# Kernel tuning notes

Measured on AMD Instinct MI355X. Metric: run time of the kernel, lower is better.

The kernel has to match this reference:

```python
import jax, jax.numpy as jnp
import numpy as np

EPS = 1e-6
N_REP = 4  # num_heads // num_kv_heads


def _qk_norm(a):
    a32 = a.astype(jnp.float32)
    var = jnp.mean(jnp.square(a32), axis=-1, keepdims=True)
    return (a32 * jax.lax.rsqrt(var + EPS)).astype(a.dtype)


def setup_inputs() -> dict:
    key = jax.random.key(0)
    ks = jax.random.split(key, 5)
    B, Tq, C, H, D, Hkv = 2, 2048, 2048, 16, 128, 4
    s = 0.02
    return {
        "x_q": jax.random.normal(ks[0], (B, Tq, C), dtype=jnp.float32),
        "Wq": jax.random.normal(ks[1], (C, H, D), dtype=jnp.float32) * s,
        "Wk": jax.random.normal(ks[2], (C, Hkv, D), dtype=jnp.float32) * s,
        "Wv": jax.random.normal(ks[3], (C, Hkv, D), dtype=jnp.float32) * s,
        "Wo": jax.random.normal(ks[4], (H * D, C), dtype=jnp.float32) * s,
    }


def reference(x_q, Wq, Wk, Wv, Wo):
    # x_q: (B, Tq, C); self-attention (x_kv = x_q)
    B, Tq, C = x_q.shape
    D = Wq.shape[-1]
    q = jnp.einsum('btc,chd->bthd', x_q, Wq)   # (B,Tq,H,D)
    k = jnp.einsum('btc,chd->bthd', x_q, Wk)   # (B,Tq,Hkv,D)
    v = jnp.einsum('btc,chd->bthd', x_q, Wv)
    # per-head QK RMS-norm
    q = _qk_norm(q)
    k = _qk_norm(k)
    # GQA: repeat kv heads (each kv head repeated N_REP times consecutively)
    k = jnp.repeat(k, N_REP, axis=2)           # (B,Tq,H,D)
    v = jnp.repeat(v, N_REP, axis=2)
    scale = jnp.asarray(1.0 / np.sqrt(D), dtype=q.dtype)
    logits = jnp.einsum('bqhd,bkhd->bhqk', q, k) * scale
    attn = jax.nn.softmax(logits, axis=-1)
    out = jnp.einsum('bhqk,bkhd->bqhd', attn, v)
    out = out.reshape(B, Tq, -1)               # (B,Tq,H*D)
    return out @ Wo                            # (B,Tq,C)
```

## Files before the change

### kernel.cpp

```cpp
#include <hip/hip_runtime.h>

typedef __attribute__((ext_vector_type(4))) float f32x4;
typedef __attribute__((ext_vector_type(16))) float f32x16;
typedef __attribute__((ext_vector_type(8))) short bf16x8;
typedef __attribute__((ext_vector_type(4))) unsigned u32x4;

#define DEV __device__ __forceinline__

DEV unsigned short f2bf(float f) {
  unsigned u = __float_as_uint(f);
  unsigned r = (u + 0x7FFFu + ((u >> 16) & 1u)) >> 16;
  return (unsigned short)r;
}
DEV float bf2f(unsigned short h) { return __uint_as_float(((unsigned)h) << 16); }

DEV unsigned cvtpk(float lo, float hi) {
  unsigned r;
  asm("v_cvt_pk_bf16_f32 %0, %1, %2" : "=v"(r) : "v"(lo), "v"(hi));
  return r;
}
DEV bf16x8 frag4(unsigned a, unsigned b, unsigned c, unsigned d) {
  u32x4 u = {a, b, c, d};
  return __builtin_bit_cast(bf16x8, u);
}

typedef __attribute__((address_space(1))) void gas_t;
typedef __attribute__((address_space(3))) void las_t;
DEV void async16(void* lds, const void* g) {
  __builtin_amdgcn_global_load_lds((gas_t*)g, (las_t*)lds, 16, 0, 0);
}

__global__ void cast_x(const float* __restrict__ x, unsigned short* __restrict__ y, int n8) {
  int idx = blockIdx.x * blockDim.x + threadIdx.x;
  int stride = gridDim.x * blockDim.x;
  for (; idx < n8; idx += stride) {
    const float4* p = (const float4*)(x + (size_t)idx * 8);
    float4 v0 = p[0], v1 = p[1];
    bf16x8 o;
    o[0] = (short)f2bf(v0.x); o[1] = (short)f2bf(v0.y);
    o[2] = (short)f2bf(v0.z); o[3] = (short)f2bf(v0.w);
    o[4] = (short)f2bf(v1.x); o[5] = (short)f2bf(v1.y);
    o[6] = (short)f2bf(v1.z); o[7] = (short)f2bf(v1.w);
    *(bf16x8*)(y + (size_t)idx * 8) = o;
  }
}

__global__ void transpose_cast(const float* __restrict__ W, unsigned short* __restrict__ Wt,
                               int Kdim, int Nw) {
  __shared__ float tile[32][33];
  int n0 = blockIdx.x * 32, k0 = blockIdx.y * 32;
  int tx = threadIdx.x, ty = threadIdx.y;
#pragma unroll
  for (int r = ty; r < 32; r += 8)
    tile[r][tx] = W[(size_t)(k0 + r) * Nw + n0 + tx];
  __syncthreads();
#pragma unroll
  for (int r = ty; r < 32; r += 8)
    Wt[(size_t)(n0 + r) * Kdim + k0 + tx] = f2bf(tile[tx][r]);
}

template <int EPI>
__global__ __launch_bounds__(256, 3)
void gemm_bt(const unsigned short* __restrict__ A, const unsigned short* __restrict__ Bt,
             int Kr, float* __restrict__ Cf, int Nr,
             unsigned short* __restrict__ Qn, unsigned short* __restrict__ Kn,
             unsigned short* __restrict__ Vt, float qscale) {
  __shared__ __align__(16) unsigned short lsA[128 * 32];
  __shared__ __align__(16) unsigned short lsB[128 * 32];
  const int t = threadIdx.x;
  const int lane = t & 63;
  const int w = t >> 6, wr = w >> 1, wc = w & 1;
  const int lo = lane & 15, hi = lane >> 4;
  const int nwg = gridDim.x * 32;
  const int bid0 = blockIdx.y * gridDim.x + blockIdx.x;
  const int sw = (bid0 & 7) * (nwg >> 3) + (bid0 >> 3);
  const int m0 = (sw & 31) * 128, n0 = (sw >> 5) * 128;

  const int c0 = t, c1 = t + 256;
  const unsigned short* gA0 = A + (size_t)(m0 + (c0 >> 2)) * Kr + (c0 & 3) * 8;
  const unsigned short* gA1 = A + (size_t)(m0 + (c1 >> 2)) * Kr + (c1 & 3) * 8;
  const unsigned short* gB0 = Bt + (size_t)(n0 + (c0 >> 2)) * Kr + (c0 & 3) * 8;
  const unsigned short* gB1 = Bt + (size_t)(n0 + (c1 >> 2)) * Kr + (c1 & 3) * 8;
  unsigned short* lA0 = lsA + c0 * 8;
  unsigned short* lA1 = lsA + c1 * 8;
  unsigned short* lB0 = lsB + c0 * 8;
  unsigned short* lB1 = lsB + c1 * 8;

  f32x4 acc[4][4] = {};

  for (int kt = 0; kt < Kr; kt += 32) {
    async16(lA0, gA0 + kt);
    async16(lA1, gA1 + kt);
    async16(lB0, gB0 + kt);
    async16(lB1, gB1 + kt);
    __syncthreads();
    bf16x8 af[4], bfr[4];
#pragma unroll
    for (int i = 0; i < 4; ++i) {
      af[i]  = *(const bf16x8*)&lsA[(wr * 64 + i * 16 + lo) * 32 + hi * 8];
      bfr[i] = *(const bf16x8*)&lsB[(wc * 64 + i * 16 + lo) * 32 + hi * 8];
    }
#pragma unroll
    for (int mi = 0; mi < 4; ++mi)
#pragma unroll
      for (int ni = 0; ni < 4; ++ni)
        acc[mi][ni] = __builtin_amdgcn_mfma_f32_16x16x32_bf16(af[mi], bfr[ni], acc[mi][ni], 0, 0, 0);
    __syncthreads();
  }

  float rr[4][4];
  if (EPI == 1 && n0 < 2560) {
    const float scl = (n0 < 2048) ? qscale : 1.0f;
    float p[4][4];
#pragma unroll
    for (int mi = 0; mi < 4; ++mi)
#pragma unroll
      for (int i = 0; i < 4; ++i) {
        float s = 0.f;
#pragma unroll
        for (int ni = 0; ni < 4; ++ni) s += acc[mi][ni][i] * acc[mi][ni][i];
        p[mi][i] = s;
      }
#pragma unroll
    for (int off = 1; off < 16; off <<= 1)
#pragma unroll
      for (int mi = 0; mi < 4; ++mi)
#pragma unroll
        for (int i = 0; i < 4; ++i) p[mi][i] += __shfl_xor(p[mi][i], off, 64);
    float* red = (float*)lsA;
    if (lo == 0)
#pragma unroll
      for (int mi = 0; mi < 4; ++mi)
#pragma unroll
        for (int i = 0; i < 4; ++i)
          red[(wr * 2 + wc) * 64 + mi * 16 + hi * 4 + i] = p[mi][i];
    __syncthreads();
#pragma unroll
    for (int mi = 0; mi < 4; ++mi)
#pragma unroll
      for (int i = 0; i < 4; ++i) {
        float tot = p[mi][i] + red[(wr * 2 + (wc ^ 1)) * 64 + mi * 16 + hi * 4 + i];
        rr[mi][i] = rsqrtf(tot * (1.0f / 128.0f) + 1e-6f) * scl;
      }
  }

#pragma unroll
  for (int mi = 0; mi < 4; ++mi)
#pragma unroll
    for (int ni = 0; ni < 4; ++ni)
#pragma unroll
      for (int i = 0; i < 4; ++i) {
        int gm = m0 + wr * 64 + mi * 16 + hi * 4 + i;
        int gn = n0 + wc * 64 + ni * 16 + lo;
        float v = acc[mi][ni][i];
        if (EPI == 0) {
          Cf[(size_t)gm * Nr + gn] = v;
        } else {
          if (n0 < 2560) v *= rr[mi][i];
          unsigned short bv = f2bf(v);
          int bb = gm >> 11, tt = gm & 2047;
          if (gn < 2048) {
            int hh = gn >> 7, dd = gn & 127;
            Qn[(((size_t)bb * 16 + hh) * 2048 + tt) * 128 + dd] = bv;
          } else if (gn < 2560) {
            int g2 = gn - 2048, hh = g2 >> 7, dd = g2 & 127;
            Kn[(((size_t)bb * 4 + hh) * 2048 + tt) * 128 + dd] = bv;
          } else {
            int g2 = gn - 2560, hh = g2 >> 7, dd = g2 & 127;
            Vt[(((size_t)bb * 4 + hh) * 128 + dd) * 2048 + tt] = bv;
          }
        }
      }
}

__global__ __launch_bounds__(256, 2)
void attn(const unsigned short* __restrict__ Q, const unsigned short* __restrict__ Kk,
          const unsigned short* __restrict__ Vt, unsigned short* __restrict__ AO) {
  const int bid = blockIdx.x;
  const int bh = (bid & 7) + 8 * (bid >> 7);
  const int qx = (bid >> 3) & 15;
  const int b = bh >> 4, h = bh & 15;
  const int hkv = h >> 2;
  const int t = threadIdx.x;
  const int w = t >> 6, lane = t & 63;
  const int qi = lane & 31, h1 = lane >> 5;
  const unsigned short* Qb = Q  + (size_t)bh * 2048 * 128;
  const unsigned short* Kb = Kk + (size_t)(b * 4 + hkv) * 2048 * 128;
  const unsigned short* Vb = Vt + (size_t)(b * 4 + hkv) * 128 * 2048;
  const int q0 = qx * 128 + w * 32;

  __shared__ __align__(16) unsigned short Klds[2][64 * 128];
  __shared__ __align__(16) unsigned short Vlds[2][128 * 64];

  bf16x8 qf[8];
#pragma unroll
  for (int s = 0; s < 8; ++s)
    qf[s] = *(const bf16x8*)&Qb[(size_t)(q0 + qi) * 128 + s * 16 + h1 * 8];

  f32x16 Oc[4] = {};
  float mrow = -1e30f, srow = 0.f;

#define STAGE_KV(bufi, kt_)                                                      \
  {                                                                              \
    const unsigned short* gK = Kb + (size_t)(kt_) * 128;                         \
    const unsigned short* gV = Vb + (kt_);                                       \
    _Pragma("unroll")                                                            \
    for (int j = 0; j < 4; ++j) {                                                \
      int gi = j * 256 + t;                                                      \
      int kr = gi >> 4, kg = (gi & 15) ^ (kr & 15);                              \
      async16(&Klds[bufi][gi * 8], gK + (size_t)kr * 128 + kg * 8);              \
      int vr = gi >> 3, vg = (gi & 7) ^ (vr & 7);                                \
      async16(&Vlds[bufi][gi * 8], gV + (size_t)vr * 2048 + vg * 8);             \
    }                                                                            \
  }

  STAGE_KV(0, 0);
  __syncthreads();

  int cur = 0;
  for (int kt = 0; kt < 2048; kt += 64) {
    if (kt + 64 < 2048) STAGE_KV(cur ^ 1, kt + 64);

    const unsigned short* KL = Klds[cur];
    const unsigned short* VL = Vlds[cur];

    f32x16 S[2] = {};
    __builtin_amdgcn_s_setprio(1);
#pragma unroll
    for (int mt = 0; mt < 2; ++mt) {
      const int krow = mt * 32 + qi;
      const unsigned short* krp = KL + krow * 128;
      const int rswz = krow & 15;
#pragma unroll
      for (int s = 0; s < 8; ++s) {
        bf16x8 kf = *(const bf16x8*)(krp + (((2 * s + h1) ^ rswz) << 3));
        S[mt] = __builtin_amdgcn_mfma_f32_32x32x16_bf16(kf, qf[s], S[mt], 0, 0, 0);
      }
    }
    __builtin_amdgcn_s_setprio(0);

    float t8[8];
#pragma unroll
    for (int r = 0; r < 8; ++r)
      t8[r] = fmaxf(fmaxf(S[0][r], S[0][r + 8]), fmaxf(S[1][r], S[1][r + 8]));
#pragma unroll
    for (int r = 0; r < 4; ++r) t8[r] = fmaxf(t8[r], t8[r + 4]);
    float mx = fmaxf(fmaxf(t8[0], t8[1]), fmaxf(t8[2], t8[3]));
    mx = fmaxf(mx, __shfl_xor(mx, 32, 64));
    if (__any(mx > mrow + 8.0f)) {
      float mnew = fmaxf(mrow, mx);
      float al = __builtin_amdgcn_exp2f(mrow - mnew);
      mrow = mnew;
      srow *= al;
#pragma unroll
      for (int dt = 0; dt < 4; ++dt)
#pragma unroll
        for (int r = 0; r < 16; ++r) Oc[dt][r] *= al;
    }
#pragma unroll
    for (int mt = 0; mt < 2; ++mt)
#pragma unroll
      for (int r = 0; r < 16; ++r)
        S[mt][r] = __builtin_amdgcn_exp2f(S[mt][r] - mrow);
    float s8[8];
#pragma unroll
    for (int r = 0; r < 8; ++r)
      s8[r] = (S[0][r] + S[0][r + 8]) + (S[1][r] + S[1][r + 8]);
#pragma unroll
    for (int r = 0; r < 4; ++r) s8[r] += s8[r + 4];
    float rs = (s8[0] + s8[1]) + (s8[2] + s8[3]);
    rs += __shfl_xor(rs, 32, 64);
    srow += rs;

    __builtin_amdgcn_s_setprio(1);
#pragma unroll
    for (int mt = 0; mt < 2; ++mt) {
      unsigned wd[8];
#pragma unroll
      for (int i2 = 0; i2 < 8; ++i2) wd[i2] = cvtpk(S[mt][2 * i2], S[mt][2 * i2 + 1]);
      unsigned r0 = __shfl_xor(h1 ? wd[0] : wd[2], 32, 64);
      unsigned r1 = __shfl_xor(h1 ? wd[1] : wd[3], 32, 64);
      unsigned r2 = __shfl_xor(h1 ? wd[4] : wd[6], 32, 64);
      unsigned r3 = __shfl_xor(h1 ? wd[5] : wd[7], 32, 64);
      bf16x8 pf0 = frag4(h1 ? r0 : wd[0], h1 ? r1 : wd[1], h1 ? wd[2] : r0, h1 ? wd[3] : r1);
      bf16x8 pf1 = frag4(h1 ? r2 : wd[4], h1 ? r3 : wd[5], h1 ? wd[6] : r2, h1 ? wd[7] : r3);
#pragma unroll
      for (int dt = 0; dt < 4; ++dt) {
        const int vrow = dt * 32 + qi;
        const unsigned short* vrp = VL + vrow * 64;
        const int vswz = vrow & 7;
        bf16x8 v0 = *(const bf16x8*)(vrp + (((mt * 4 + 0 + h1) ^ vswz) << 3));
        bf16x8 v1 = *(const bf16x8*)(vrp + (((mt * 4 + 2 + h1) ^ vswz) << 3));
        Oc[dt] = __builtin_amdgcn_mfma_f32_32x32x16_bf16(v0, pf0, Oc[dt], 0, 0, 0);
        Oc[dt] = __builtin_amdgcn_mfma_f32_32x32x16_bf16(v1, pf1, Oc[dt], 0, 0, 0);
      }
    }
    __builtin_amdgcn_s_setprio(0);

    __syncthreads();
    cur ^= 1;
  }

  const float inv = 1.0f / srow;
  const size_t orow = ((size_t)(b * 2048 + q0 + qi)) * 2048 + h * 128;
#pragma unroll
  for (int dt = 0; dt < 4; ++dt)
#pragma unroll
    for (int rq = 0; rq < 4; ++rq) {
      int d0 = dt * 32 + 8 * rq + 4 * h1;
      unsigned u0 = cvtpk(Oc[dt][4 * rq + 0] * inv, Oc[dt][4 * rq + 1] * inv);
      unsigned u1 = cvtpk(Oc[dt][4 * rq + 2] * inv, Oc[dt][4 * rq + 3] * inv);
      uint2 st = {u0, u1};
      *(uint2*)((unsigned short*)AO + orow + d0) = st;
    }
}

extern "C" void kernel_launch(void* const* d_in, const int* in_sizes, int n_in,
                              void* d_out, int out_size, void* d_ws, size_t ws_size,
                              hipStream_t stream) {
  const float* x_q = (const float*)d_in[0];
  const float* Wq  = (const float*)d_in[1];
  const float* Wk  = (const float*)d_in[2];
  const float* Wv  = (const float*)d_in[3];
  const float* Wo  = (const float*)d_in[4];
  float* out = (float*)d_out;

  char* ws = (char*)d_ws;
  unsigned short* Xb    = (unsigned short*)(ws);
  unsigned short* WqkvT = (unsigned short*)(ws + 16777216);
  unsigned short* WoT   = (unsigned short*)(ws + 29360128);
  unsigned short* Qn    = (unsigned short*)(ws + 37748736);
  unsigned short* Kn    = (unsigned short*)(ws + 54525952);
  unsigned short* Vt    = (unsigned short*)(ws + 58720256);
  unsigned short* AO    = Xb;

  cast_x<<<2048, 256, 0, stream>>>(x_q, Xb, (4096 * 2048) / 8);
  transpose_cast<<<dim3(2048 / 32, 2048 / 32), dim3(32, 8), 0, stream>>>(Wq, WqkvT, 2048, 2048);
  transpose_cast<<<dim3(512 / 32, 2048 / 32), dim3(32, 8), 0, stream>>>(Wk, WqkvT + 2048 * 2048, 2048, 512);
  transpose_cast<<<dim3(512 / 32, 2048 / 32), dim3(32, 8), 0, stream>>>(Wv, WqkvT + 2560 * 2048, 2048, 512);
  transpose_cast<<<dim3(2048 / 32, 2048 / 32), dim3(32, 8), 0, stream>>>(Wo, WoT, 2048, 2048);

  gemm_bt<1><<<dim3(3072 / 128, 4096 / 128), 256, 0, stream>>>(Xb, WqkvT, 2048, nullptr, 0,
                                                               Qn, Kn, Vt, 0.12751742f);
  attn<<<512, 256, 0, stream>>>(Qn, Kn, Vt, AO);
  gemm_bt<0><<<dim3(2048 / 128, 4096 / 128), 256, 0, stream>>>(AO, WoT, 2048, out, 2048,
                                                               nullptr, nullptr, nullptr, 0.f);
}
```

Measured before the change: 238.8 us.

## Merge prep kernels into one launch and deepen GEMM K-tile with XOR swizzle

Replaces the five cast and transpose launches with a single prep kernel that dispatches on block index, which removes per-launch overhead. The projection GEMM now stages K in chunks of 64 instead of 32, with an XOR swizzle on LDS chunk placement so fragment reads avoid bank conflicts. This halves the barrier count per K and doubles LDS use per block, which may reduce occupancy under the 3-blocks launch bound.

Result: faster. 214.3 us (median of 3 runs) (-10.3%).

```diff
diff --git a/kernel.cpp b/kernel.cpp
--- a/kernel.cpp
+++ b/kernel.cpp
@@ -30,33 +30,42 @@
   __builtin_amdgcn_global_load_lds((gas_t*)g, (las_t*)lds, 16, 0, 0);
 }
 
-__global__ void cast_x(const float* __restrict__ x, unsigned short* __restrict__ y, int n8) {
-  int idx = blockIdx.x * blockDim.x + threadIdx.x;
-  int stride = gridDim.x * blockDim.x;
-  for (; idx < n8; idx += stride) {
-    const float4* p = (const float4*)(x + (size_t)idx * 8);
-    float4 v0 = p[0], v1 = p[1];
-    bf16x8 o;
-    o[0] = (short)f2bf(v0.x); o[1] = (short)f2bf(v0.y);
-    o[2] = (short)f2bf(v0.z); o[3] = (short)f2bf(v0.w);
-    o[4] = (short)f2bf(v1.x); o[5] = (short)f2bf(v1.y);
-    o[6] = (short)f2bf(v1.z); o[7] = (short)f2bf(v1.w);
-    *(bf16x8*)(y + (size_t)idx * 8) = o;
-  }
-}
-
-__global__ void transpose_cast(const float* __restrict__ W, unsigned short* __restrict__ Wt,
-                               int Kdim, int Nw) {
+__global__ __launch_bounds__(256)
+void prep(const float* __restrict__ x, const float* __restrict__ Wq,
+          const float* __restrict__ Wk, const float* __restrict__ Wv,
+          const float* __restrict__ Wo, unsigned short* __restrict__ Xb,
+          unsigned short* __restrict__ WqkvT, unsigned short* __restrict__ WoT) {
+  const int bid = blockIdx.x, t = threadIdx.x;
+  if (bid < 512) {
+    int idx = bid * 256 + t;
+    for (; idx < 1048576; idx += 131072) {
+      const float4* p = (const float4*)(x + (size_t)idx * 8);
+      float4 v0 = p[0], v1 = p[1];
+      bf16x8 o;
+      o[0] = (short)f2bf(v0.x); o[1] = (short)f2bf(v0.y);
+      o[2] = (short)f2bf(v0.z); o[3] = (short)f2bf(v0.w);
+      o[4] = (short)f2bf(v1.x); o[5] = (short)f2bf(v1.y);
+      o[6] = (short)f2bf(v1.z); o[7] = (short)f2bf(v1.w);
+      *(bf16x8*)(Xb + (size_t)idx * 8) = o;
+    }
+    return;
+  }
+  const float* W;
+  unsigned short* Wt;
+  int n0, k0, Nw;
+  if (bid < 4608)      { int b2 = bid - 512;  W = Wq; Wt = WqkvT;              Nw = 2048; n0 = (b2 & 63) * 32; k0 = (b2 >> 6) * 32; }
+  else if (bid < 5632) { int b2 = bid - 4608; W = Wk; Wt = WqkvT + 2048 * 2048; Nw = 512;  n0 = (b2 & 15) * 32; k0 = (b2 >> 4) * 32; }
+  else if (bid < 6656) { int b2 = bid - 5632; W = Wv; Wt = WqkvT + 2560 * 2048; Nw = 512;  n0 = (b2 & 15) * 32; k0 = (b2 >> 4) * 32; }
+  else                 { int b2 = bid - 6656; W = Wo; Wt = WoT;                Nw = 2048; n0 = (b2 & 63) * 32; k0 = (b2 >> 6) * 32; }
   __shared__ float tile[32][33];
-  int n0 = blockIdx.x * 32, k0 = blockIdx.y * 32;
-  int tx = threadIdx.x, ty = threadIdx.y;
+  const int tx = t & 31, ty = t >> 5;
 #pragma unroll
   for (int r = ty; r < 32; r += 8)
     tile[r][tx] = W[(size_t)(k0 + r) * Nw + n0 + tx];
   __syncthreads();
 #pragma unroll
   for (int r = ty; r < 32; r += 8)
-    Wt[(size_t)(n0 + r) * Kdim + k0 + tx] = f2bf(tile[tx][r]);
+    Wt[(size_t)(n0 + r) * 2048 + k0 + tx] = f2bf(tile[tx][r]);
 }
 
 template <int EPI>
@@ -65,46 +74,43 @@
              int Kr, float* __restrict__ Cf, int Nr,
              unsigned short* __restrict__ Qn, unsigned short* __restrict__ Kn,
              unsigned short* __restrict__ Vt, float qscale) {
-  __shared__ __align__(16) unsigned short lsA[128 * 32];
-  __shared__ __align__(16) unsigned short lsB[128 * 32];
+  __shared__ __align__(16) unsigned short lsA[128 * 64];
+  __shared__ __align__(16) unsigned short lsB[128 * 64];
   const int t = threadIdx.x;
   const int lane = t & 63;
   const int w = t >> 6, wr = w >> 1, wc = w & 1;
   const int lo = lane & 15, hi = lane >> 4;
+  const int swz = lo & 7;
   const int nwg = gridDim.x * 32;
   const int bid0 = blockIdx.y * gridDim.x + blockIdx.x;
   const int sw = (bid0 & 7) * (nwg >> 3) + (bid0 >> 3);
   const int m0 = (sw & 31) * 128, n0 = (sw >> 5) * 128;
 
-  const int c0 = t, c1 = t + 256;
-  const unsigned short* gA0 = A + (size_t)(m0 + (c0 >> 2)) * Kr + (c0 & 3) * 8;
-  const unsigned short* gA1 = A + (size_t)(m0 + (c1 >> 2)) * Kr + (c1 & 3) * 8;
-  const unsigned short* gB0 = Bt + (size_t)(n0 + (c0 >> 2)) * Kr + (c0 & 3) * 8;
-  const unsigned short* gB1 = Bt + (size_t)(n0 + (c1 >> 2)) * Kr + (c1 & 3) * 8;
-  unsigned short* lA0 = lsA + c0 * 8;
-  unsigned short* lA1 = lsA + c1 * 8;
-  unsigned short* lB0 = lsB + c0 * 8;
-  unsigned short* lB1 = lsB + c1 * 8;
-
   f32x4 acc[4][4] = {};
 
-  for (int kt = 0; kt < Kr; kt += 32) {
-    async16(lA0, gA0 + kt);
-    async16(lA1, gA1 + kt);
-    async16(lB0, gB0 + kt);
-    async16(lB1, gB1 + kt);
+  for (int kt = 0; kt < Kr; kt += 64) {
+#pragma unroll
+    for (int j = 0; j < 4; ++j) {
+      int gi = j * 256 + t;
+      int rw = gi >> 3, g = (gi & 7) ^ (rw & 7);
+      async16(lsA + gi * 8, A + (size_t)(m0 + rw) * Kr + kt + g * 8);
+      async16(lsB + gi * 8, Bt + (size_t)(n0 + rw) * Kr + kt + g * 8);
+    }
     __syncthreads();
-    bf16x8 af[4], bfr[4];
-#pragma unroll
-    for (int i = 0; i < 4; ++i) {
-      af[i]  = *(const bf16x8*)&lsA[(wr * 64 + i * 16 + lo) * 32 + hi * 8];
-      bfr[i] = *(const bf16x8*)&lsB[(wc * 64 + i * 16 + lo) * 32 + hi * 8];
-    }
-#pragma unroll
-    for (int mi = 0; mi < 4; ++mi)
-#pragma unroll
-      for (int ni = 0; ni < 4; ++ni)
-        acc[mi][ni] = __builtin_amdgcn_mfma_f32_16x16x32_bf16(af[mi], bfr[ni], acc[mi][ni], 0, 0, 0);
+#pragma unroll
+    for (int kk = 0; kk < 2; ++kk) {
+      bf16x8 af[4], bfr[4];
+#pragma unroll
+      for (int i = 0; i < 4; ++i) {
+        af[i]  = *(const bf16x8*)&lsA[(wr * 64 + i * 16 + lo) * 64 + (((kk * 4 + hi) ^ swz) << 3)];
+        bfr[i] = *(const bf16x8*)&lsB[(wc * 64 + i * 16 + lo) * 64 + (((kk * 4 + hi) ^ swz) << 3)];
+      }
+#pragma unroll
+      for (int mi = 0; mi < 4; ++mi)
+#pragma unroll
+        for (int ni = 0; ni < 4; ++ni)
+          acc[mi][ni] = __builtin_amdgcn_mfma_f32_16x16x32_bf16(af[mi], bfr[ni], acc[mi][ni], 0, 0, 0);
+    }
     __syncthreads();
   }
 
@@ -334,11 +340,7 @@
   unsigned short* Vt    = (unsigned short*)(ws + 58720256);
   unsigned short* AO    = Xb;
 
-  cast_x<<<2048, 256, 0, stream>>>(x_q, Xb, (4096 * 2048) / 8);
-  transpose_cast<<<dim3(2048 / 32, 2048 / 32), dim3(32, 8), 0, stream>>>(Wq, WqkvT, 2048, 2048);
-  transpose_cast<<<dim3(512 / 32, 2048 / 32), dim3(32, 8), 0, stream>>>(Wk, WqkvT + 2048 * 2048, 2048, 512);
-  transpose_cast<<<dim3(512 / 32, 2048 / 32), dim3(32, 8), 0, stream>>>(Wv, WqkvT + 2560 * 2048, 2048, 512);
-  transpose_cast<<<dim3(2048 / 32, 2048 / 32), dim3(32, 8), 0, stream>>>(Wo, WoT, 2048, 2048);
+  prep<<<10752, 256, 0, stream>>>(x_q, Wq, Wk, Wv, Wo, Xb, WqkvT, WoT);
 
   gemm_bt<1><<<dim3(3072 / 128, 4096 / 128), 256, 0, stream>>>(Xb, WqkvT, 2048, nullptr, 0,
                                                                Qn, Kn, Vt, 0.12751742f);
```
